# Kernel tuning notes

Hardware: AMD Instinct MI355X
Metric: run time of the kernel (lower is better)

## Reference

```python
import jax, jax.numpy as jnp
import numpy as np
from functools import partial

B, T, H, K = 64, 256, 200, 48
START_TAG, END_TAG = 46, 47


def setup_inputs() -> dict:
    key = jax.random.key(0)
    k1, k2, k3 = jax.random.split(key, 3)
    feats = jax.random.normal(k1, (B, T, H), dtype=jnp.float32)
    W_e = jax.random.normal(k2, (K, H), dtype=jnp.float32) * (6.0 / (K + H)) ** 0.5
    b_e = jnp.zeros((K,), dtype=jnp.float32)
    targets = jax.random.randint(k3, (B, T), 0, K * K, dtype=jnp.int64)
    mask = jnp.ones((B, T), dtype=jnp.int32)
    return {"feats": feats, "W_e": W_e, "b_e": b_e, "targets": targets,
            "mask": mask, "start_tag": START_TAG, "end_tag": END_TAG}


def reference(feats, W_e, b_e, targets, mask, start_tag, end_tag):
    # feats: [B,T,H]; emission: [B,T,K]
    emission = jnp.einsum('bth,kh->btk', feats, W_e) + b_e
    Bs, Ts, Ks = emission.shape
    lengths = mask.sum(-1)  # [B]
    valid = jnp.arange(Ts)[None, :] < lengths[:, None]  # [B,T]

    # crf_scores[b,t,i,j] = emission[b,t,j] (unsqueeze(2).expand). Gather at
    # flattened index targets = i*K + j picks emission[b,t, targets % K].
    gold_per_t = jnp.take_along_axis(emission, (targets % Ks)[..., None], axis=2)[..., 0]
    gold_score = jnp.sum(jnp.where(valid, gold_per_t, 0.0), axis=1)  # [B]

    # Forward algorithm. t=0: scores_upto_t = scores[:,0,start_tag,:] = emission[:,0,:]
    s0 = jnp.where((lengths > 0)[:, None], emission[:, 0, :], 0.0)  # [B,K]

    def step(s, xs):
        em_t, active = xs  # em_t: [B,K], active: [B]
        # scores[b,t,i,j] + s[b,i], logsumexp over i (prev tag)
        new = jax.scipy.special.logsumexp(em_t[:, None, :] + s[:, :, None], axis=1)
        s = jnp.where(active[:, None], new, s)
        return s, None

    xs = (jnp.swapaxes(emission[:, 1:, :], 0, 1), jnp.swapaxes(valid[:, 1:], 0, 1))
    s_final, _ = jax.lax.scan(step, s0, xs)

    all_paths_scores = s_final[:, end_tag]  # [B]
    viterbi_loss = all_paths_scores - gold_score
    return viterbi_loss
```

## Files before the change

kernel.cpp:

```cpp
#include <hip/hip_runtime.h>
#include <hip/hip_bf16.h>

#define BB 64
#define TT 256
#define HH 200
#define KK 48
#define C4 50
#define AS 216

typedef __attribute__((ext_vector_type(8))) short bf16x8;
typedef __attribute__((ext_vector_type(4))) float f32x4;

static __device__ __forceinline__ unsigned short f2bf(float x) {
    __hip_bfloat16 h = __float2bfloat16(x);
    return *reinterpret_cast<unsigned short*>(&h);
}

__global__ __launch_bounds__(256)
void crf_mfma_kernel(const float* __restrict__ feats,
                     const float* __restrict__ W_e,
                     const float* __restrict__ b_e,
                     const int*   __restrict__ targets,
                     const int*   __restrict__ mask,
                     const int*   __restrict__ end_tag_p,
                     float*       __restrict__ out)
{
    __shared__ __align__(16) unsigned short Albs[64 * AS];
    __shared__ __align__(16) unsigned short Wlds[48 * AS];
    __shared__ float wpart[4];

    const int tid  = threadIdx.x;
    const int lane = tid & 63;
    const int w    = tid >> 6;
    const int bidx = blockIdx.x >> 2;
    const int tq   = blockIdx.x & 3;

    {
        const float4* f4 = reinterpret_cast<const float4*>(feats) +
                           (size_t)(bidx * TT + tq * 64) * C4;
        for (int i = tid; i < 64 * C4; i += 256) {
            const int r = i / C4, cc = i - r * C4;
            const float4 v = f4[i];
            ushort4 o = { f2bf(v.x), f2bf(v.y), f2bf(v.z), f2bf(v.w) };
            *reinterpret_cast<ushort4*>(&Albs[r * AS + cc * 4]) = o;
        }
        const float4* w4 = reinterpret_cast<const float4*>(W_e);
        for (int i = tid; i < KK * C4; i += 256) {
            const int r = i / C4, cc = i - r * C4;
            const float4 v = w4[i];
            ushort4 o = { f2bf(v.x), f2bf(v.y), f2bf(v.z), f2bf(v.w) };
            *reinterpret_cast<ushort4*>(&Wlds[r * AS + cc * 4]) = o;
        }
    }

    int len;
    {
        const int4 mv4 = reinterpret_cast<const int4*>(mask + bidx * TT)[lane];
        int mv = mv4.x + mv4.y + mv4.z + mv4.w;
        #pragma unroll
        for (int off = 32; off >= 1; off >>= 1) mv += __shfl_xor(mv, off);
        len = mv;
    }
    __syncthreads();

    const int rg = lane >> 4;
    const int cc = lane & 15;

    const unsigned short* Ap  = &Albs[(w * 16 + cc) * AS];
    const unsigned short* Bp0 = &Wlds[(0  + cc) * AS];
    const unsigned short* Bp1 = &Wlds[(16 + cc) * AS];
    const unsigned short* Bp2 = &Wlds[(32 + cc) * AS];

    f32x4 ac0 = {0.f, 0.f, 0.f, 0.f};
    f32x4 ac1 = {0.f, 0.f, 0.f, 0.f};
    f32x4 ac2 = {0.f, 0.f, 0.f, 0.f};

    #pragma unroll
    for (int kc = 0; kc < 7; ++kc) {
        const int koff = kc * 32 + rg * 8;
        bf16x8 a, b0, b1, b2;
        if (kc < 6 || rg == 0) {
            a  = *reinterpret_cast<const bf16x8*>(Ap  + koff);
            b0 = *reinterpret_cast<const bf16x8*>(Bp0 + koff);
            b1 = *reinterpret_cast<const bf16x8*>(Bp1 + koff);
            b2 = *reinterpret_cast<const bf16x8*>(Bp2 + koff);
        } else {
            a = (bf16x8)(short)0; b0 = a; b1 = a; b2 = a;
        }
        ac0 = __builtin_amdgcn_mfma_f32_16x16x32_bf16(a, b0, ac0, 0, 0, 0);
        ac1 = __builtin_amdgcn_mfma_f32_16x16x32_bf16(a, b1, ac1, 0, 0, 0);
        ac2 = __builtin_amdgcn_mfma_f32_16x16x32_bf16(a, b2, ac2, 0, 0, 0);
    }

    const float bb0 = b_e[cc], bb1 = b_e[16 + cc], bb2 = b_e[32 + cc];
    const int   ET  = end_tag_p[0];

    float csum = 0.0f;
    #pragma unroll
    for (int j = 0; j < 4; ++j) {
        const float x0 = ac0[j] + bb0;
        const float x1 = ac1[j] + bb1;
        const float x2 = ac2[j] + bb2;

        const int r  = w * 16 + rg * 4 + j;
        const int gt = tq * 64 + r;
        const int tg = targets[bidx * TT + gt] % KK;

        float mx = fmaxf(fmaxf(x0, x1), x2);
        #pragma unroll
        for (int off = 8; off >= 1; off >>= 1) mx = fmaxf(mx, __shfl_xor(mx, off));
        float s = expf(x0 - mx) + expf(x1 - mx) + expf(x2 - mx);
        float g = ((0  + cc) == tg ? x0 : 0.f) + ((16 + cc) == tg ? x1 : 0.f)
                + ((32 + cc) == tg ? x2 : 0.f);
        float e = ((0  + cc) == ET ? x0 : 0.f) + ((16 + cc) == ET ? x1 : 0.f)
                + ((32 + cc) == ET ? x2 : 0.f);
        #pragma unroll
        for (int off = 8; off >= 1; off >>= 1) {
            s += __shfl_xor(s, off);
            g += __shfl_xor(g, off);
            e += __shfl_xor(e, off);
        }
        const float lse = mx + logf(s);

        float cr = 0.0f;
        if (gt < len)          cr -= g;
        if (gt == len - 1)     cr += e;
        else if (gt < len - 1) cr += lse;
        csum += cr;
    }

    float v = (cc == 0) ? csum : 0.0f;
    v += __shfl_xor(v, 16);
    v += __shfl_xor(v, 32);
    if (lane == 0) wpart[w] = v;
    __syncthreads();
    if (tid == 0) {
        atomicAdd(out + bidx, wpart[0] + wpart[1] + wpart[2] + wpart[3]);
    }
}

extern "C" void kernel_launch(void* const* d_in, const int* in_sizes, int n_in,
                              void* d_out, int out_size, void* d_ws, size_t ws_size,
                              hipStream_t stream) {
    const float* feats   = (const float*)d_in[0];
    const float* W_e     = (const float*)d_in[1];
    const float* b_e     = (const float*)d_in[2];
    const int*   targets = (const int*)d_in[3];
    const int*   mask    = (const int*)d_in[4];
    const int*   et      = (const int*)d_in[6];
    float*       out     = (float*)d_out;

    hipMemsetAsync(out, 0, BB * sizeof(float), stream);
    crf_mfma_kernel<<<dim3(BB * 4), dim3(256), 0, stream>>>(
        feats, W_e, b_e, targets, mask, et, out);
}
```

Before: 79.16 us.

## Load feats directly into MFMA B-fragments and transpose output mapping

Drops the LDS staging of the feats tile: each lane reads its time-step row straight from global memory, converts it to bf16 and feeds it to the MFMA as the B operand, with W_e as the A operand from LDS. This swaps the output layout so that each lane column holds one time step, which lets the logsumexp and gold/end-tag selection run mostly in registers with fewer cross-lane shuffles. The block-level shared reduction and barrier are replaced by per-wave atomics. Global feats loads become strided per lane (one row of 800 bytes per lane), which may coalesce less well than the previous cooperative float4 loads.

```diff
diff --git a/kernel.cpp b/kernel.cpp
--- a/kernel.cpp
+++ b/kernel.cpp
@@ -5,7 +5,6 @@
 #define TT 256
 #define HH 200
 #define KK 48
-#define C4 50
 #define AS 216
 
 typedef __attribute__((ext_vector_type(8))) short bf16x8;
@@ -17,17 +16,15 @@
 }
 
 __global__ __launch_bounds__(256)
-void crf_mfma_kernel(const float* __restrict__ feats,
-                     const float* __restrict__ W_e,
-                     const float* __restrict__ b_e,
-                     const int*   __restrict__ targets,
-                     const int*   __restrict__ mask,
-                     const int*   __restrict__ end_tag_p,
-                     float*       __restrict__ out)
+void crf_one(const float* __restrict__ feats,
+             const float* __restrict__ W_e,
+             const float* __restrict__ b_e,
+             const int*   __restrict__ targets,
+             const int*   __restrict__ mask,
+             const int*   __restrict__ end_tag_p,
+             float*       __restrict__ out)
 {
-    __shared__ __align__(16) unsigned short Albs[64 * AS];
-    __shared__ __align__(16) unsigned short Wlds[48 * AS];
-    __shared__ float wpart[4];
+    __shared__ __align__(16) unsigned short Wlds[KK * AS];
 
     const int tid  = threadIdx.x;
     const int lane = tid & 63;
@@ -36,20 +33,12 @@
     const int tq   = blockIdx.x & 3;
 
     {
-        const float4* f4 = reinterpret_cast<const float4*>(feats) +
-                           (size_t)(bidx * TT + tq * 64) * C4;
-        for (int i = tid; i < 64 * C4; i += 256) {
-            const int r = i / C4, cc = i - r * C4;
-            const float4 v = f4[i];
-            ushort4 o = { f2bf(v.x), f2bf(v.y), f2bf(v.z), f2bf(v.w) };
-            *reinterpret_cast<ushort4*>(&Albs[r * AS + cc * 4]) = o;
-        }
         const float4* w4 = reinterpret_cast<const float4*>(W_e);
-        for (int i = tid; i < KK * C4; i += 256) {
-            const int r = i / C4, cc = i - r * C4;
+        for (int i = tid; i < KK * 50; i += 256) {
+            const int r = i / 50, c = i - r * 50;
             const float4 v = w4[i];
             ushort4 o = { f2bf(v.x), f2bf(v.y), f2bf(v.z), f2bf(v.w) };
-            *reinterpret_cast<ushort4*>(&Wlds[r * AS + cc * 4]) = o;
+            *reinterpret_cast<ushort4*>(&Wlds[r * AS + c * 4]) = o;
         }
     }
 
@@ -65,78 +54,81 @@
 
     const int rg = lane >> 4;
     const int cc = lane & 15;
+    const int tb = tq * 64 + w * 16;
+    const int gt = tb + cc;
 
-    const unsigned short* Ap  = &Albs[(w * 16 + cc) * AS];
-    const unsigned short* Bp0 = &Wlds[(0  + cc) * AS];
-    const unsigned short* Bp1 = &Wlds[(16 + cc) * AS];
-    const unsigned short* Bp2 = &Wlds[(32 + cc) * AS];
+    const float* frow = feats + (size_t)(bidx * TT + gt) * HH;
 
-    f32x4 ac0 = {0.f, 0.f, 0.f, 0.f};
-    f32x4 ac1 = {0.f, 0.f, 0.f, 0.f};
-    f32x4 ac2 = {0.f, 0.f, 0.f, 0.f};
+    f32x4 ac0 = {0.f,0.f,0.f,0.f}, ac1 = {0.f,0.f,0.f,0.f}, ac2 = {0.f,0.f,0.f,0.f};
 
     #pragma unroll
     for (int kc = 0; kc < 7; ++kc) {
-        const int koff = kc * 32 + rg * 8;
-        bf16x8 a, b0, b1, b2;
+        const int h0 = kc * 32 + rg * 8;
+        bf16x8 bfr, a0, a1, a2;
         if (kc < 6 || rg == 0) {
-            a  = *reinterpret_cast<const bf16x8*>(Ap  + koff);
-            b0 = *reinterpret_cast<const bf16x8*>(Bp0 + koff);
-            b1 = *reinterpret_cast<const bf16x8*>(Bp1 + koff);
-            b2 = *reinterpret_cast<const bf16x8*>(Bp2 + koff);
+            const float4 v0 = *reinterpret_cast<const float4*>(frow + h0);
+            const float4 v1 = *reinterpret_cast<const float4*>(frow + h0 + 4);
+            bfr[0]=(short)f2bf(v0.x); bfr[1]=(short)f2bf(v0.y);
+            bfr[2]=(short)f2bf(v0.z); bfr[3]=(short)f2bf(v0.w);
+            bfr[4]=(short)f2bf(v1.x); bfr[5]=(short)f2bf(v1.y);
+            bfr[6]=(short)f2bf(v1.z); bfr[7]=(short)f2bf(v1.w);
+            a0 = *reinterpret_cast<const bf16x8*>(&Wlds[( 0 + cc) * AS + h0]);
+            a1 = *reinterpret_cast<const bf16x8*>(&Wlds[(16 + cc) * AS + h0]);
+            a2 = *reinterpret_cast<const bf16x8*>(&Wlds[(32 + cc) * AS + h0]);
         } else {
-            a = (bf16x8)(short)0; b0 = a; b1 = a; b2 = a;
+            bfr = (bf16x8)(short)0; a0 = bfr; a1 = bfr; a2 = bfr;
         }
-        ac0 = __builtin_amdgcn_mfma_f32_16x16x32_bf16(a, b0, ac0, 0, 0, 0);
-        ac1 = __builtin_amdgcn_mfma_f32_16x16x32_bf16(a, b1, ac1, 0, 0, 0);
-        ac2 = __builtin_amdgcn_mfma_f32_16x16x32_bf16(a, b2, ac2, 0, 0, 0);
+        ac0 = __builtin_amdgcn_mfma_f32_16x16x32_bf16(a0, bfr, ac0, 0, 0, 0);
+        ac1 = __builtin_amdgcn_mfma_f32_16x16x32_bf16(a1, bfr, ac1, 0, 0, 0);
+        ac2 = __builtin_amdgcn_mfma_f32_16x16x32_bf16(a2, bfr, ac2, 0, 0, 0);
     }
 
-    const float bb0 = b_e[cc], bb1 = b_e[16 + cc], bb2 = b_e[32 + cc];
-    const int   ET  = end_tag_p[0];
+    const float4 bq0 = *reinterpret_cast<const float4*>(b_e +  0 + rg * 4);
+    const float4 bq1 = *reinterpret_cast<const float4*>(b_e + 16 + rg * 4);
+    const float4 bq2 = *reinterpret_cast<const float4*>(b_e + 32 + rg * 4);
+    float x[12];
+    x[0]=ac0[0]+bq0.x; x[1]=ac0[1]+bq0.y; x[2] =ac0[2]+bq0.z; x[3] =ac0[3]+bq0.w;
+    x[4]=ac1[0]+bq1.x; x[5]=ac1[1]+bq1.y; x[6] =ac1[2]+bq1.z; x[7] =ac1[3]+bq1.w;
+    x[8]=ac2[0]+bq2.x; x[9]=ac2[1]+bq2.y; x[10]=ac2[2]+bq2.z; x[11]=ac2[3]+bq2.w;
 
-    float csum = 0.0f;
+    const int ET  = end_tag_p[0];
+    const int tgt = targets[bidx * TT + gt] % KK;
+
+    float m = x[0];
     #pragma unroll
-    for (int j = 0; j < 4; ++j) {
-        const float x0 = ac0[j] + bb0;
-        const float x1 = ac1[j] + bb1;
-        const float x2 = ac2[j] + bb2;
-
-        const int r  = w * 16 + rg * 4 + j;
-        const int gt = tq * 64 + r;
-        const int tg = targets[bidx * TT + gt] % KK;
-
-        float mx = fmaxf(fmaxf(x0, x1), x2);
-        #pragma unroll
-        for (int off = 8; off >= 1; off >>= 1) mx = fmaxf(mx, __shfl_xor(mx, off));
-        float s = expf(x0 - mx) + expf(x1 - mx) + expf(x2 - mx);
-        float g = ((0  + cc) == tg ? x0 : 0.f) + ((16 + cc) == tg ? x1 : 0.f)
-                + ((32 + cc) == tg ? x2 : 0.f);
-        float e = ((0  + cc) == ET ? x0 : 0.f) + ((16 + cc) == ET ? x1 : 0.f)
-                + ((32 + cc) == ET ? x2 : 0.f);
-        #pragma unroll
-        for (int off = 8; off >= 1; off >>= 1) {
-            s += __shfl_xor(s, off);
-            g += __shfl_xor(g, off);
-            e += __shfl_xor(e, off);
-        }
-        const float lse = mx + logf(s);
-
-        float cr = 0.0f;
-        if (gt < len)          cr -= g;
-        if (gt == len - 1)     cr += e;
-        else if (gt < len - 1) cr += lse;
-        csum += cr;
+    for (int i = 1; i < 12; ++i) m = fmaxf(m, x[i]);
+    float s = 0.f, g = 0.f, e = 0.f;
+    #pragma unroll
+    for (int i = 0; i < 12; ++i) {
+        s += expf(x[i] - m);
+        const int q = i >> 2;
+        const int kk = q * 16 + rg * 4 + (i & 3);
+        g += (kk == tgt) ? x[i] : 0.f;
+        e += (kk == ET)  ? x[i] : 0.f;
     }
 
-    float v = (cc == 0) ? csum : 0.0f;
-    v += __shfl_xor(v, 16);
-    v += __shfl_xor(v, 32);
-    if (lane == 0) wpart[w] = v;
-    __syncthreads();
-    if (tid == 0) {
-        atomicAdd(out + bidx, wpart[0] + wpart[1] + wpart[2] + wpart[3]);
+    #pragma unroll
+    for (int off = 16; off <= 32; off <<= 1) {
+        const float om = __shfl_xor(m, off);
+        const float os = __shfl_xor(s, off);
+        const float nm = fmaxf(m, om);
+        s = s * expf(m - nm) + os * expf(om - nm);
+        m = nm;
+        g += __shfl_xor(g, off);
+        e += __shfl_xor(e, off);
     }
+    const float lse = m + logf(s);
+
+    float c = 0.0f;
+    if (gt < len)          c -= g;
+    if (gt == len - 1)     c += e;
+    else if (gt < len - 1) c += lse;
+    if (rg != 0) c = 0.0f;
+
+    #pragma unroll
+    for (int off = 8; off >= 1; off >>= 1) c += __shfl_xor(c, off);
+    c += __shfl_xor(c, 16); c += __shfl_xor(c, 32);
+    if (lane == 0) atomicAdd(out + bidx, c);
 }
 
 extern "C" void kernel_launch(void* const* d_in, const int* in_sizes, int n_in,
@@ -151,6 +143,6 @@
     float*       out     = (float*)d_out;
 
     hipMemsetAsync(out, 0, BB * sizeof(float), stream);
-    crf_mfma_kernel<<<dim3(BB * 4), dim3(256), 0, stream>>>(
+    crf_one<<<dim3(BB * 4), dim3(256), 0, stream>>>(
         feats, W_e, b_e, targets, mask, et, out);
 }
```

Measured after the change: 83.25 us. 1.05x slower.
